# Kernel optimization log

Measured on AMD Instinct MI355X. Metric: run time of the kernel, lower is better.

## Reference

```python
import jax, jax.numpy as jnp
import numpy as np

B, D, L, TABLE, C, HID = 32768, 8, 16, 524288, 2, 512
GROWTH = 1.3
_PRIMES = [2654436881, 5915587277, 1500450271, 3267000013, 5754853343, 4093082899, 9576890767, 3628273133]
# torch mixes int64/int32 with python-int scalars; only the low 32 bits matter for
# mod-by-power-of-two table_size, so int32 wraparound arithmetic is bit-exact here.
PRIMES32 = jnp.asarray(np.array([p % (1 << 32) for p in _PRIMES], dtype=np.uint64).astype(np.uint32).view(np.int32))


def _linear_init(key, out_f, in_f):
    s = 1.0 / np.sqrt(in_f)
    kw, kb = jax.random.split(key)
    w = jax.random.uniform(kw, (out_f, in_f), jnp.float32, -s, s)
    b = jax.random.uniform(kb, (out_f,), jnp.float32, -s, s)
    return w, b


def setup_inputs() -> dict:
    key = jax.random.key(0)
    ks = jax.random.split(key, 6)
    x = jax.random.normal(ks[0], (B, D), jnp.float32)
    T = jax.random.normal(ks[1], (L, TABLE, C), jnp.float32)
    K = jnp.power(jnp.float32(GROWTH), jnp.arange(L, dtype=jnp.float32))[:, None]  # [L,1]
    l1_w, l1_b = _linear_init(ks[2], HID, D + L * C)
    l2_w, l2_b = _linear_init(ks[3], HID, HID)
    act_w, act_b = _linear_init(ks[4], 4, HID)
    val_w, val_b = _linear_init(ks[5], 1, HID)
    return dict(x=x, T=T, K=K, l1_w=l1_w, l1_b=l1_b, l2_w=l2_w, l2_b=l2_b,
                act_w=act_w, act_b=act_b, val_w=val_w, val_b=val_b)


def reference(x, T, K, l1_w, l1_b, l2_w, l2_b, act_w, act_b, val_w, val_b):
    Bn, Dn = x.shape
    Ln, table_size, Cn = T.shape
    p = jnp.cumsum(x, -1)[:, None, :] * K                      # [B,L,D]
    frac = p - jnp.trunc(p)                                    # torch.frac semantics (sign of p)
    c = jnp.sort(frac, -1)                                     # [B,L,D]
    R = (frac[..., None] >= c[..., None, :]).astype(x.dtype)   # [B,L,D,D]
    R = jnp.concatenate([R, jnp.zeros(R.shape[:-1] + (1,), x.dtype)], -1)  # [B,L,D,D+1]
    c = jnp.concatenate([c, jnp.ones(c.shape[:-1] + (1,), x.dtype)], -1)   # [B,L,D+1]
    A = R + jnp.floor(p)[..., None]                            # [B,L,D,D+1]
    A = A - jnp.concatenate([jnp.zeros_like(A[..., :1, :]), A[..., :-1, :]], -2)
    c = c - jnp.concatenate([jnp.zeros_like(c[..., :1]), c[..., :-1]], -1)
    Ai = A.astype(jnp.int32)                                   # trunc toward zero, like .int()
    terms = Ai * PRIMES32[None, None, :Dn, None]               # int32 wraparound multiply
    cidx = terms[:, :, 0]
    for i in range(1, Dn):                                     # small fixed D, XOR chain
        cidx = jnp.bitwise_xor(cidx, terms[:, :, i])           # [B,L,D+1]
    idx = jnp.mod(cidx, table_size)                            # floor-mod -> non-negative
    f = T[jnp.arange(Ln)[None, :, None], idx]                  # gather -> [B,L,D+1,C]
    f = (f * c[..., None] / K[:, :, None]).sum(2)              # [B,L,C]
    h = jnp.concatenate([x, f.reshape(Bn, -1)], -1)            # [B, D + L*C]
    h = jax.nn.relu(h @ l1_w.T + l1_b)
    h = jax.nn.relu(h @ l2_w.T + l2_b)
    action = h @ act_w.T + act_b                               # [B,4]
    value = h @ val_w.T + val_b                                # [B,1]
    return action, value
```

## Files before the change

### kernel.cpp

```cpp
#include <hip/hip_runtime.h>
#include <cstdint>
#include <cstddef>

#define BB   32768
#define DD   8
#define LLV  16
#define TBL  524288
#define HID  512

typedef __attribute__((ext_vector_type(8))) short short8;
typedef __attribute__((ext_vector_type(8))) unsigned short u16x8;
typedef __attribute__((ext_vector_type(4))) float f32x4;
typedef __attribute__((ext_vector_type(2))) float f32x2;

__device__ __constant__ uint32_t PR[8] = {
    2654436881u, 1620619981u, 1500450271u, 3267000013u,
    1459886047u, 4093082899u,  986956175u, 3628273133u
};

__device__ __forceinline__ unsigned short f2bf(float f) {
    uint32_t u = __float_as_uint(f);
    uint32_t r = (u + 0x7fffu + ((u >> 16) & 1u)) >> 16;
    return (unsigned short)r;
}

__device__ __forceinline__ void enc_idx(const float xs[8], float Kl,
                                        uint32_t idx9[9], float w9[9])
{
    float fr[8];
    int   base[8];
    float cs = 0.f;
#pragma unroll
    for (int i2 = 0; i2 < 8; i2++) {
        cs += xs[i2];
        float p = cs * Kl;
        fr[i2]   = p - truncf(p);
        base[i2] = (int)floorf(p);
    }

    float c[8];
#pragma unroll
    for (int i2 = 0; i2 < 8; i2++) c[i2] = fr[i2];
#define CE(a_, b_) { float lo_ = fminf(c[a_], c[b_]); float hi_ = fmaxf(c[a_], c[b_]); c[a_] = lo_; c[b_] = hi_; }
    CE(0,1) CE(2,3) CE(4,5) CE(6,7)
    CE(0,2) CE(1,3) CE(4,6) CE(5,7)
    CE(1,2) CE(5,6) CE(0,4) CE(3,7)
    CE(1,5) CE(2,6)
    CE(1,4) CE(3,6)
    CE(2,4) CE(3,5)
    CE(3,4)
#undef CE

    float prevc = 0.f;
#pragma unroll
    for (int j = 0; j < 9; j++) {
        float cj = (j < 8) ? c[j] : 1.0f;
        uint32_t h = 0;
        int prev = 0;
#pragma unroll
        for (int i2 = 0; i2 < 8; i2++) {
            int ai = base[i2] + (fr[i2] >= cj ? 1 : 0);
            h ^= (uint32_t)(ai - prev) * PR[i2];
            prev = ai;
        }
        idx9[j] = h & (TBL - 1);
        w9[j]   = cj - prevc;
        prevc   = cj;
    }
}

__global__ __launch_bounds__(256) void k_encode(
    const float* __restrict__ x, const float* __restrict__ T,
    const float* __restrict__ Karr, unsigned short* __restrict__ h0T,
    const float* __restrict__ w2, unsigned short* __restrict__ w2p,
    const float* __restrict__ w1, unsigned short* __restrict__ w1p)
{
    int i = blockIdx.x;
    if (i >= 2048) {
        int bid2 = i - 2048;
        if (bid2 < 128) {
            int u  = bid2 * 256 + threadIdx.x;
            int kg = u & 3, kc = (u >> 2) & 15, c = u >> 6;
            const float* src = w2 + (size_t)c * 512 + kc * 32 + kg * 8;
            unsigned short fr[8];
#pragma unroll
            for (int e = 0; e < 8; ++e) fr[e] = f2bf(src[e]);
            *(u16x8*)(w2p + ((((size_t)kc * 512 + c) * 4 + kg) << 3)) = *(u16x8*)fr;
        } else {
            int u  = (bid2 - 128) * 256 + threadIdx.x;
            int kg = u & 3, ks = (u >> 2) & 1, c = u >> 3;
            int kbase = ks * 32 + kg * 8;
            unsigned short fr[8];
#pragma unroll
            for (int e = 0; e < 8; ++e) {
                int k = kbase + e;
                fr[e] = (k < 40) ? f2bf(w1[(size_t)c * 40 + k]) : (unsigned short)0;
            }
            *(u16x8*)(w1p + ((((size_t)ks * 512 + c) * 4 + kg) << 3)) = *(u16x8*)fr;
        }
        return;
    }

    int l = (i & 7) + ((i >> 10) << 3);
    int b = ((i & 1023) >> 3) * 256 + threadIdx.x;

    const float4 x0 = *(const float4*)(x + (size_t)b * DD);
    const float4 x1 = *(const float4*)(x + (size_t)b * DD + 4);
    float xs[8] = {x0.x, x0.y, x0.z, x0.w, x1.x, x1.y, x1.z, x1.w};

    float Kl = Karr[l];
    const f32x2* Tl = (const f32x2*)(T + ((size_t)l * TBL) * 2);

    uint32_t idx9[9];
    float    w9[9];
    enc_idx(xs, Kl, idx9, w9);

    f32x2 t0, t1, t2, t3, t4, t5, t6, t7, t8;
#define GL(n) asm volatile("global_load_dwordx2 %0, %1, off" \
                           : "=v"(t##n) : "v"(Tl + idx9[n]));
    GL(0) GL(1) GL(2) GL(3) GL(4) GL(5) GL(6) GL(7) GL(8)
#undef GL
    asm volatile("s_waitcnt vmcnt(0)"
        : "+v"(t0), "+v"(t1), "+v"(t2), "+v"(t3), "+v"(t4),
          "+v"(t5), "+v"(t6), "+v"(t7), "+v"(t8));
    __builtin_amdgcn_sched_barrier(0);

    float f0, f1;
    f0 = t0[0] * w9[0];  f1 = t0[1] * w9[0];
    f0 = fmaf(t1[0], w9[1], f0); f1 = fmaf(t1[1], w9[1], f1);
    f0 = fmaf(t2[0], w9[2], f0); f1 = fmaf(t2[1], w9[2], f1);
    f0 = fmaf(t3[0], w9[3], f0); f1 = fmaf(t3[1], w9[3], f1);
    f0 = fmaf(t4[0], w9[4], f0); f1 = fmaf(t4[1], w9[4], f1);
    f0 = fmaf(t5[0], w9[5], f0); f1 = fmaf(t5[1], w9[5], f1);
    f0 = fmaf(t6[0], w9[6], f0); f1 = fmaf(t6[1], w9[6], f1);
    f0 = fmaf(t7[0], w9[7], f0); f1 = fmaf(t7[1], w9[7], f1);
    f0 = fmaf(t8[0], w9[8], f0); f1 = fmaf(t8[1], w9[8], f1);
    f0 /= Kl;
    f1 /= Kl;

    h0T[(size_t)(l * 2 + 0) * BB + b] = f2bf(f0);
    h0T[(size_t)(l * 2 + 1) * BB + b] = f2bf(f1);
}

__global__ __launch_bounds__(512, 2) void k_fused(
    const unsigned short* __restrict__ h0T, const float* __restrict__ x,
    const unsigned short* __restrict__ w1p, const unsigned short* __restrict__ w2p,
    const float* __restrict__ b1, const float* __restrict__ b2,
    const float* __restrict__ aw, const float* __restrict__ ab,
    const float* __restrict__ vw, const float* __restrict__ vb,
    float* __restrict__ out)
{
    __shared__ unsigned short h1s[128 * 512];
    __shared__ unsigned short h0s[128 * 64];

    const int tid  = threadIdx.x;
    const int wid  = tid >> 6;
    const int lane = tid & 63;
    const int wm = wid >> 2, wn = wid & 3;
    const int lr = lane & 15;
    const int kg = lane >> 4;
    const int b0 = blockIdx.x * 128;

    {
        int p = tid >> 4, c = tid & 15;
        u16x8 v = *(const u16x8*)(h0T + (size_t)p * BB + b0 + c * 8);
#pragma unroll
        for (int e = 0; e < 8; ++e) {
            int row = c * 8 + e;
            int byte = ((row << 7) + (8 + p) * 2) ^ ((row & 7) << 4);
            *(unsigned short*)((char*)h0s + byte) = v[e];
        }
        if (tid < 128) {
            int row = tid;
            const float4 x0 = *(const float4*)(x + (size_t)(b0 + row) * 8);
            const float4 x1 = *(const float4*)(x + (size_t)(b0 + row) * 8 + 4);
            unsigned short xv[8] = {
                f2bf(x0.x), f2bf(x0.y), f2bf(x0.z), f2bf(x0.w),
                f2bf(x1.x), f2bf(x1.y), f2bf(x1.z), f2bf(x1.w)};
            *(u16x8*)((char*)h0s + ((row << 7) ^ ((row & 7) << 4))) = *(u16x8*)xv;
        } else {
            int t2 = tid - 128;
            int row = t2 / 3, seg = t2 - row * 3;
            int byte = ((row << 7) + 80 + seg * 16) ^ ((row & 7) << 4);
            u16x8 z = {0, 0, 0, 0, 0, 0, 0, 0};
            *(u16x8*)((char*)h0s + byte) = z;
        }
    }
    __syncthreads();

    f32x4 acc[4][8];
#pragma unroll
    for (int m = 0; m < 4; ++m)
#pragma unroll
        for (int n = 0; n < 8; ++n) acc[m][n] = (f32x4){0.f, 0.f, 0.f, 0.f};

#pragma unroll
    for (int ks = 0; ks < 2; ++ks) {
        int kbyte = ks * 64 + kg * 16;
        short8 af[4];
#pragma unroll
        for (int m = 0; m < 4; ++m) {
            int row = wm * 64 + m * 16 + lr;
            int a = ((row << 7) + kbyte) ^ ((row & 7) << 4);
            af[m] = *(const short8*)((const char*)h0s + a);
        }
        short8 bfr[8];
#pragma unroll
        for (int n = 0; n < 8; ++n) {
            int col = wn * 128 + n * 16 + lr;
            bfr[n] = *(const short8*)(w1p + ((((size_t)ks * 512 + col) * 4 + kg) << 3));
        }
#pragma unroll
        for (int m = 0; m < 4; ++m)
#pragma unroll
            for (int n = 0; n < 8; ++n)
                acc[m][n] = __builtin_amdgcn_mfma_f32_16x16x32_bf16(
                    af[m], bfr[n], acc[m][n], 0, 0, 0);
    }

    short8 aX[4], bX[8], aY[4], bY[8];

#define LDA(dst, kc)                                                            \
    _Pragma("unroll")                                                           \
    for (int m = 0; m < 4; ++m) {                                               \
        int row = wm * 64 + m * 16 + lr;                                        \
        int a = (((row << 10) + (kc) * 64 + kg * 16)) ^ ((row & 7) << 4);       \
        dst[m] = *(const short8*)((const char*)h1s + a);                        \
    }
#define LDB(dst, kc)                                                            \
    _Pragma("unroll")                                                           \
    for (int n = 0; n < 8; ++n) {                                               \
        int col = wn * 128 + n * 16 + lr;                                       \
        dst[n] = *(const short8*)(w2p + ((((size_t)(kc) * 512 + col) * 4 + kg) << 3)); \
    }
#define MM(aa, bb)                                                              \
    __builtin_amdgcn_sched_barrier(0);                                          \
    __builtin_amdgcn_s_setprio(1);                                              \
    _Pragma("unroll")                                                           \
    for (int m = 0; m < 4; ++m)                                                 \
        _Pragma("unroll")                                                       \
        for (int n = 0; n < 8; ++n)                                             \
            acc[m][n] = __builtin_amdgcn_mfma_f32_16x16x32_bf16(                \
                aa[m], bb[n], acc[m][n], 0, 0, 0);                              \
    __builtin_amdgcn_s_setprio(0);

    LDB(bX, 0)
    LDB(bY, 1)
#pragma unroll
    for (int n = 0; n < 8; ++n) {
        int col = wn * 128 + n * 16 + lr;
        float b1v = b1[col];
#pragma unroll
        for (int m = 0; m < 4; ++m) {
#pragma unroll
            for (int r = 0; r < 4; ++r) {
                int row = wm * 64 + m * 16 + kg * 4 + r;
                int byte = ((row << 10) + col * 2) ^ ((row & 7) << 4);
                *(unsigned short*)((char*)h1s + byte) =
                    f2bf(fmaxf(acc[m][n][r] + b1v, 0.f));
            }
        }
    }
    __syncthreads();

#pragma unroll
    for (int m = 0; m < 4; ++m)
#pragma unroll
        for (int n = 0; n < 8; ++n) acc[m][n] = (f32x4){0.f, 0.f, 0.f, 0.f};

    LDA(aX, 0)
    LDA(aY, 1)              MM(aX, bX)
    LDA(aX, 2)  LDB(bX, 2)  MM(aY, bY)
    LDA(aY, 3)  LDB(bY, 3)  MM(aX, bX)
    LDA(aX, 4)  LDB(bX, 4)  MM(aY, bY)
    LDA(aY, 5)  LDB(bY, 5)  MM(aX, bX)
    LDA(aX, 6)  LDB(bX, 6)  MM(aY, bY)
    LDA(aY, 7)  LDB(bY, 7)  MM(aX, bX)
    LDA(aX, 8)  LDB(bX, 8)  MM(aY, bY)
    LDA(aY, 9)  LDB(bY, 9)  MM(aX, bX)
    LDA(aX, 10) LDB(bX, 10) MM(aY, bY)
    LDA(aY, 11) LDB(bY, 11) MM(aX, bX)
    LDA(aX, 12) LDB(bX, 12) MM(aY, bY)
    LDA(aY, 13) LDB(bY, 13) MM(aX, bX)
    LDA(aX, 14) LDB(bX, 14) MM(aY, bY)
    LDA(aY, 15) LDB(bY, 15) MM(aX, bX)
    MM(aY, bY)
#undef LDA
#undef LDB
#undef MM

#pragma unroll
    for (int n = 0; n < 8; ++n) {
        int col = wn * 128 + n * 16 + lr;
        float b2v = b2[col];
#pragma unroll
        for (int m = 0; m < 4; ++m)
#pragma unroll
            for (int r = 0; r < 4; ++r)
                acc[m][n][r] = fmaxf(acc[m][n][r] + b2v, 0.f);
    }

    float hwv[5][8];
#pragma unroll
    for (int n = 0; n < 8; ++n) {
        int col = wn * 128 + n * 16 + lr;
        hwv[0][n] = aw[col];
        hwv[1][n] = aw[512 + col];
        hwv[2][n] = aw[1024 + col];
        hwv[3][n] = aw[1536 + col];
        hwv[4][n] = vw[col];
    }
    float* spart = (float*)h0s;
#pragma unroll
    for (int hm = 0; hm < 5; ++hm) {
        f32x4 p[4];
#pragma unroll
        for (int m = 0; m < 4; ++m) {
            p[m] = acc[m][0] * hwv[hm][0];
#pragma unroll
            for (int n = 1; n < 8; ++n) p[m] += acc[m][n] * hwv[hm][n];
        }
#pragma unroll
        for (int d = 1; d < 16; d <<= 1)
#pragma unroll
            for (int m = 0; m < 4; ++m)
#pragma unroll
                for (int r = 0; r < 4; ++r)
                    p[m][r] += __shfl_xor(p[m][r], d);
        if (lr == 0) {
#pragma unroll
            for (int m = 0; m < 4; ++m)
#pragma unroll
                for (int r = 0; r < 4; ++r)
                    spart[(wn * 5 + hm) * 128 + wm * 64 + m * 16 + kg * 4 + r] = p[m][r];
        }
    }
    __syncthreads();

    if (tid < 128) {
        int b = b0 + tid;
        float s[5];
#pragma unroll
        for (int hm = 0; hm < 5; ++hm) {
            float v = spart[(0 * 5 + hm) * 128 + tid] + spart[(1 * 5 + hm) * 128 + tid]
                    + spart[(2 * 5 + hm) * 128 + tid] + spart[(3 * 5 + hm) * 128 + tid];
            s[hm] = v;
        }
        float4 act = make_float4(s[0] + ab[0], s[1] + ab[1], s[2] + ab[2], s[3] + ab[3]);
        *(float4*)(out + (size_t)b * 4) = act;
        out[(size_t)BB * 4 + b] = s[4] + vb[0];
    }
}

extern "C" void kernel_launch(void* const* d_in, const int* in_sizes, int n_in,
                              void* d_out, int out_size, void* d_ws, size_t ws_size,
                              hipStream_t stream)
{
    const float* x    = (const float*)d_in[0];
    const float* T    = (const float*)d_in[1];
    const float* K    = (const float*)d_in[2];
    const float* l1w  = (const float*)d_in[3];
    const float* l1b  = (const float*)d_in[4];
    const float* l2w  = (const float*)d_in[5];
    const float* l2b  = (const float*)d_in[6];
    const float* actw = (const float*)d_in[7];
    const float* actb = (const float*)d_in[8];
    const float* valw = (const float*)d_in[9];
    const float* valb = (const float*)d_in[10];
    float* out = (float*)d_out;

    char* ws = (char*)d_ws;
    unsigned short* h0T = (unsigned short*)ws;
    unsigned short* w2p = (unsigned short*)(ws + 2097152);
    unsigned short* w1p = (unsigned short*)(ws + 2621440);

    k_encode <<<2192, 256, 0, stream>>>(x, T, K, h0T, l2w, w2p, l1w, w1p);
    k_fused  <<<256, 512, 0, stream>>>(h0T, x, w1p, w2p, l1b, l2b,
                                       actw, actb, valw, valb, out);
}
```

Measured before the change: 60.98 us.

## Retile layer-2 GEMM so each warp covers all rows and a 64-column slice

The layer-2 MFMA tiling changes from a 2x4 warp grid (64 rows x 128 cols per warp) to 8 warps that each own all 128 rows and a 64-column slice. Each W2 column fragment is now fetched from global/L2 by one warp instead of two, halving redundant weight traffic, while LDS reads of the activation tile double per warp. The head reduction is adapted to 8 column groups and moves to h1s behind an extra barrier. This trades global load pressure for LDS bandwidth and one more sync.

```diff
diff --git a/kernel.cpp b/kernel.cpp
--- a/kernel.cpp
+++ b/kernel.cpp
@@ -188,11 +188,11 @@
     }
     __syncthreads();
 
-    f32x4 acc[4][8];
+    f32x4 acc1[4][8];
 #pragma unroll
     for (int m = 0; m < 4; ++m)
 #pragma unroll
-        for (int n = 0; n < 8; ++n) acc[m][n] = (f32x4){0.f, 0.f, 0.f, 0.f};
+        for (int n = 0; n < 8; ++n) acc1[m][n] = (f32x4){0.f, 0.f, 0.f, 0.f};
 
 #pragma unroll
     for (int ks = 0; ks < 2; ++ks) {
@@ -214,32 +214,32 @@
         for (int m = 0; m < 4; ++m)
 #pragma unroll
             for (int n = 0; n < 8; ++n)
-                acc[m][n] = __builtin_amdgcn_mfma_f32_16x16x32_bf16(
-                    af[m], bfr[n], acc[m][n], 0, 0, 0);
-    }
-
-    short8 aX[4], bX[8], aY[4], bY[8];
+                acc1[m][n] = __builtin_amdgcn_mfma_f32_16x16x32_bf16(
+                    af[m], bfr[n], acc1[m][n], 0, 0, 0);
+    }
+
+    short8 aX[8], bX[4], aY[8], bY[4];
 
 #define LDA(dst, kc)                                                            \
     _Pragma("unroll")                                                           \
-    for (int m = 0; m < 4; ++m) {                                               \
-        int row = wm * 64 + m * 16 + lr;                                        \
+    for (int m = 0; m < 8; ++m) {                                               \
+        int row = m * 16 + lr;                                                  \
         int a = (((row << 10) + (kc) * 64 + kg * 16)) ^ ((row & 7) << 4);       \
         dst[m] = *(const short8*)((const char*)h1s + a);                        \
     }
 #define LDB(dst, kc)                                                            \
     _Pragma("unroll")                                                           \
-    for (int n = 0; n < 8; ++n) {                                               \
-        int col = wn * 128 + n * 16 + lr;                                       \
+    for (int n = 0; n < 4; ++n) {                                               \
+        int col = wid * 64 + n * 16 + lr;                                       \
         dst[n] = *(const short8*)(w2p + ((((size_t)(kc) * 512 + col) * 4 + kg) << 3)); \
     }
 #define MM(aa, bb)                                                              \
     __builtin_amdgcn_sched_barrier(0);                                          \
     __builtin_amdgcn_s_setprio(1);                                              \
     _Pragma("unroll")                                                           \
-    for (int m = 0; m < 4; ++m)                                                 \
+    for (int m = 0; m < 8; ++m)                                                 \
         _Pragma("unroll")                                                       \
-        for (int n = 0; n < 8; ++n)                                             \
+        for (int n = 0; n < 4; ++n)                                             \
             acc[m][n] = __builtin_amdgcn_mfma_f32_16x16x32_bf16(                \
                 aa[m], bb[n], acc[m][n], 0, 0, 0);                              \
     __builtin_amdgcn_s_setprio(0);
@@ -257,16 +257,17 @@
                 int row = wm * 64 + m * 16 + kg * 4 + r;
                 int byte = ((row << 10) + col * 2) ^ ((row & 7) << 4);
                 *(unsigned short*)((char*)h1s + byte) =
-                    f2bf(fmaxf(acc[m][n][r] + b1v, 0.f));
+                    f2bf(fmaxf(acc1[m][n][r] + b1v, 0.f));
             }
         }
     }
     __syncthreads();
 
-#pragma unroll
-    for (int m = 0; m < 4; ++m)
-#pragma unroll
-        for (int n = 0; n < 8; ++n) acc[m][n] = (f32x4){0.f, 0.f, 0.f, 0.f};
+    f32x4 acc[8][4];
+#pragma unroll
+    for (int m = 0; m < 8; ++m)
+#pragma unroll
+        for (int n = 0; n < 4; ++n) acc[m][n] = (f32x4){0.f, 0.f, 0.f, 0.f};
 
     LDA(aX, 0)
     LDA(aY, 1)              MM(aX, bX)
@@ -290,49 +291,51 @@
 #undef MM
 
 #pragma unroll
-    for (int n = 0; n < 8; ++n) {
-        int col = wn * 128 + n * 16 + lr;
+    for (int n = 0; n < 4; ++n) {
+        int col = wid * 64 + n * 16 + lr;
         float b2v = b2[col];
 #pragma unroll
-        for (int m = 0; m < 4; ++m)
+        for (int m = 0; m < 8; ++m)
 #pragma unroll
             for (int r = 0; r < 4; ++r)
                 acc[m][n][r] = fmaxf(acc[m][n][r] + b2v, 0.f);
     }
 
-    float hwv[5][8];
-#pragma unroll
-    for (int n = 0; n < 8; ++n) {
-        int col = wn * 128 + n * 16 + lr;
+    float hwv[5][4];
+#pragma unroll
+    for (int n = 0; n < 4; ++n) {
+        int col = wid * 64 + n * 16 + lr;
         hwv[0][n] = aw[col];
         hwv[1][n] = aw[512 + col];
         hwv[2][n] = aw[1024 + col];
         hwv[3][n] = aw[1536 + col];
         hwv[4][n] = vw[col];
     }
-    float* spart = (float*)h0s;
+    __syncthreads();
+    float* spart = (float*)h1s;
 #pragma unroll
     for (int hm = 0; hm < 5; ++hm) {
-        f32x4 p[4];
-#pragma unroll
-        for (int m = 0; m < 4; ++m) {
+        f32x4 p[8];
+#pragma unroll
+        for (int m = 0; m < 8; ++m) {
             p[m] = acc[m][0] * hwv[hm][0];
-#pragma unroll
-            for (int n = 1; n < 8; ++n) p[m] += acc[m][n] * hwv[hm][n];
+            p[m] += acc[m][1] * hwv[hm][1];
+            p[m] += acc[m][2] * hwv[hm][2];
+            p[m] += acc[m][3] * hwv[hm][3];
         }
 #pragma unroll
         for (int d = 1; d < 16; d <<= 1)
 #pragma unroll
-            for (int m = 0; m < 4; ++m)
+            for (int m = 0; m < 8; ++m)
 #pragma unroll
                 for (int r = 0; r < 4; ++r)
                     p[m][r] += __shfl_xor(p[m][r], d);
         if (lr == 0) {
 #pragma unroll
-            for (int m = 0; m < 4; ++m)
+            for (int m = 0; m < 8; ++m)
 #pragma unroll
                 for (int r = 0; r < 4; ++r)
-                    spart[(wn * 5 + hm) * 128 + wm * 64 + m * 16 + kg * 4 + r] = p[m][r];
+                    spart[(wid * 5 + hm) * 128 + m * 16 + kg * 4 + r] = p[m][r];
         }
     }
     __syncthreads();
@@ -342,8 +345,9 @@
         float s[5];
 #pragma unroll
         for (int hm = 0; hm < 5; ++hm) {
-            float v = spart[(0 * 5 + hm) * 128 + tid] + spart[(1 * 5 + hm) * 128 + tid]
-                    + spart[(2 * 5 + hm) * 128 + tid] + spart[(3 * 5 + hm) * 128 + tid];
+            float v = 0.f;
+#pragma unroll
+            for (int g = 0; g < 8; ++g) v += spart[(g * 5 + hm) * 128 + tid];
             s[hm] = v;
         }
         float4 act = make_float4(s[0] + ab[0], s[1] + ab[1], s[2] + ab[2], s[3] + ab[3]);
```

After: 63.82 us. 4.7% more time.
